# Kernel tuning notes

Hardware: AMD Instinct MI355X
Metric: run time of the kernel (lower is better)

Reference implementation:

```python
import jax, jax.numpy as jnp
import numpy as np

TAU = 0.5

def setup_inputs() -> dict:
    key = jax.random.key(0)
    ks = jax.random.split(key, 8)
    B_Nq, B_Ns, C, H, W = 16, 16, 512, 32, 32
    f_q = jax.random.normal(ks[0], (B_Nq, C, H, W), dtype=jnp.float32)
    f_s = jax.random.normal(ks[1], (B_Ns, C, H, W), dtype=jnp.float32)
    # depthwise 1x1 convs with groups=dim, bias=False -> per-channel scalar weights [C]
    w_cca_q = jax.random.normal(ks[2], (C,), dtype=jnp.float32)
    w_cca_k = jax.random.normal(ks[3], (C,), dtype=jnp.float32)
    w_cca_v = jax.random.normal(ks[4], (C,), dtype=jnp.float32)
    w_sca_q = jax.random.normal(ks[5], (C,), dtype=jnp.float32)
    w_sca_k = jax.random.normal(ks[6], (C,), dtype=jnp.float32)
    lam = jnp.float32(0.1)
    return {"f_q": f_q, "f_s": f_s, "w_cca_q": w_cca_q, "w_cca_k": w_cca_k,
            "w_cca_v": w_cca_v, "w_sca_q": w_sca_q, "w_sca_k": w_sca_k, "lam": lam}

def _dw(x, w):
    # depthwise 1x1 conv, no bias == per-channel scale; x: [B,C,H,W], w: [C]
    return x * w[None, :, None, None]

def reference(f_q, f_s, w_cca_q, w_cca_k, w_cca_v, w_sca_q, w_sca_k, lam):
    B_Nq, C, H, W = f_q.shape
    B_Ns = f_s.shape[0]
    P = H * W
    qc = _dw(f_q, w_cca_q).reshape(B_Nq, C, P)          # [B,C,P]
    kc_mean = _dw(f_s, w_cca_k).reshape(B_Ns, C, P).mean(axis=0)  # [C,P]
    vc_mean = _dw(f_s, w_cca_v).reshape(B_Ns, C, P).mean(axis=0)  # [C,P]
    # channel attention: [B,C,C]
    Ac = jax.nn.softmax(jnp.einsum('bcp,dp->bcd', qc, kc_mean) / P, axis=-1)
    f_cca_q = jnp.einsum('bcd,dp->bcp', Ac, vc_mean).reshape(B_Nq, C, H, W)
    qs = _dw(f_cca_q, w_sca_q).reshape(B_Nq, C, P)      # [B,C,P]
    ks_mean = _dw(f_s, w_sca_k).reshape(B_Ns, C, P).mean(axis=0)  # [C,P]
    # spatial affinity: [B,P,P]
    M = jnp.einsum('bcp,cq->bpq', qs, ks_mean) / (TAU * C)
    alpha = jax.nn.softmax(M.mean(axis=-1), axis=-1)    # [B_Nq,P]
    beta = jax.nn.softmax(M.mean(axis=-2), axis=-1)     # [B_Nq,P]
    beta_mean = jnp.broadcast_to(beta.mean(axis=0, keepdims=True), (B_Ns, P))
    Fq_out = f_q + lam * f_cca_q
    return (Fq_out, alpha, beta_mean)
```

## Files before the change

### kernel.cpp

```cpp
#include <hip/hip_runtime.h>

typedef __bf16 bf16;
typedef __bf16 bf16x4 __attribute__((ext_vector_type(4)));
typedef __bf16 bf16x8 __attribute__((ext_vector_type(8)));
typedef float f32x4 __attribute__((ext_vector_type(4)));


#define GLL16(g, l)                                                             \
    __builtin_amdgcn_global_load_lds((const __attribute__((address_space(1))) void*)(g), \
                                     (__attribute__((address_space(3))) void*)(l), 16, 0, 0)

__device__ inline float wave_reduce_sum(float v) {
#pragma unroll
    for (int m = 32; m >= 1; m >>= 1) v += __shfl_xor(v, m, 64);
    return v;
}
__device__ inline float wave_reduce_max(float v) {
#pragma unroll
    for (int m = 32; m >= 1; m >>= 1) v = fmaxf(v, __shfl_xor(v, m, 64));
    return v;
}

__global__ void k_prep(const float* __restrict__ fs, const float* __restrict__ fq,
                       float* __restrict__ fsm32, bf16* __restrict__ fsm16,
                       bf16* __restrict__ fsmT, bf16* __restrict__ fq16) {
    __shared__ bf16 tile[32][33];
    int bx = blockIdx.x, by = blockIdx.y;
    int p0 = bx * 32, c0 = by * 32;
    int t = threadIdx.x, tx = t & 31, ty = t >> 5;
#pragma unroll
    for (int i = 0; i < 4; ++i) {
        size_t off = (size_t)(c0 + ty + 8 * i) * 1024 + p0 + tx;
        float s = 0.f;
#pragma unroll
        for (int b = 0; b < 16; ++b) s += fs[(size_t)b * 524288 + off];
        s *= (1.f / 16.f);
        fsm32[off] = s;
        bf16 h = (bf16)s;
        fsm16[off] = h;
        tile[ty + 8 * i][tx] = h;
    }
    __syncthreads();
#pragma unroll
    for (int i = 0; i < 4; ++i)
        fsmT[(size_t)(p0 + ty + 8 * i) * 512 + c0 + tx] = tile[tx][ty + 8 * i];
    int blk = by * 32 + bx;
    const float4* f4 = (const float4*)fq;
#pragma unroll
    for (int i = 0; i < 16; ++i) {
        int idx = blk * 4096 + i * 256 + t;
        float4 v = f4[idx];
        bf16x4 h4 = {(bf16)v.x, (bf16)v.y, (bf16)v.z, (bf16)v.w};
        *(bf16x4*)(fq16 + (size_t)idx * 4) = h4;
    }
}

__global__ void k_u(const float* __restrict__ fsm32, const float* __restrict__ wsq,
                    const float* __restrict__ wsk, float* __restrict__ u,
                    float* __restrict__ rm) {
    int c = blockIdx.x;
    int t = threadIdx.x;
    float s = 0.f;
#pragma unroll
    for (int j = 0; j < 4; ++j) s += fsm32[(size_t)c * 1024 + t + 256 * j];
    s = wave_reduce_sum(s);
    __shared__ float red[4];
    int w = t >> 6, lane = t & 63;
    if (lane == 0) red[w] = s;
    __syncthreads();
    if (t == 0) {
        float rmv = (red[0] + red[1] + red[2] + red[3]) * (1.f / 1024.f);
        rm[c] = rmv;
        u[c] = wsq[c] * wsk[c] * rmv * (1.f / 256.f);
    }
}

__global__ void k_gemm1(const bf16* __restrict__ A, const bf16* __restrict__ B,
                        float* __restrict__ G) {
    __shared__ alignas(16) bf16 As[64 * 32];
    __shared__ alignas(16) bf16 Bs[128 * 32];
    const int dt = blockIdx.x, ct = blockIdx.y, b = blockIdx.z;
    const int t = threadIdx.x, w = t >> 6, lane = t & 63;
    const int quad = lane >> 4, r15 = lane & 15;
    const bf16* Abase = A + ((size_t)(b * 512 + ct * 64)) * 1024;
    const bf16* Bbase = B + ((size_t)(dt * 128)) * 1024;
    const int sr = t >> 2, sc = (t & 3) * 8;
    f32x4 acc[8] = {};
    for (int k0 = 0; k0 < 1024; k0 += 32) {
        GLL16(Abase + (size_t)sr * 1024 + k0 + sc, As + t * 8);
        GLL16(Bbase + (size_t)sr * 1024 + k0 + sc, Bs + t * 8);
        GLL16(Bbase + (size_t)(sr + 64) * 1024 + k0 + sc, Bs + (t + 256) * 8);
        __syncthreads();
        bf16x8 af = *(const bf16x8*)(As + (w * 16 + r15) * 32 + quad * 8);
#pragma unroll
        for (int j = 0; j < 8; ++j) {
            bf16x8 bfr = *(const bf16x8*)(Bs + (j * 16 + r15) * 32 + quad * 8);
            acc[j] = __builtin_amdgcn_mfma_f32_16x16x32_bf16(af, bfr, acc[j], 0, 0, 0);
        }
        __syncthreads();
    }
    float* g = G + ((size_t)(b * 512 + ct * 64 + w * 16 + quad * 4)) * 512 + dt * 128 + r15;
#pragma unroll
    for (int j = 0; j < 8; ++j)
#pragma unroll
        for (int ii = 0; ii < 4; ++ii)
            g[(size_t)ii * 512 + j * 16] = acc[j][ii];
}

__global__ void k_softmax_ac(const float* __restrict__ G, const float* __restrict__ wq,
                             const float* __restrict__ wk, const float* __restrict__ wv,
                             const float* __restrict__ rm, bf16* __restrict__ Acw,
                             float* __restrict__ r) {
    int row = blockIdx.x * 4 + (threadIdx.x >> 6);
    int lane = threadIdx.x & 63;
    int c = row & 511;
    const float* g = G + (size_t)row * 512;
    float sc = wq[c] * (1.f / 1024.f);
    float v[8];
    float mx = -3.4e38f;
#pragma unroll
    for (int j = 0; j < 8; ++j) {
        int d = lane + 64 * j;
        v[j] = g[d] * sc * wk[d];
        mx = fmaxf(mx, v[j]);
    }
    mx = wave_reduce_max(mx);
    float sum = 0.f;
#pragma unroll
    for (int j = 0; j < 8; ++j) {
        v[j] = __expf(v[j] - mx);
        sum += v[j];
    }
    sum = wave_reduce_sum(sum);
    float inv = 1.f / sum;
    bf16* o = Acw + (size_t)row * 512;
    float rsum = 0.f;
#pragma unroll
    for (int j = 0; j < 8; ++j) {
        int d = lane + 64 * j;
        float aw = v[j] * inv * wv[d];
        o[d] = (bf16)aw;
        rsum += aw * rm[d];
    }
    rsum = wave_reduce_sum(rsum);
    if (lane == 0) r[row] = rsum;
}

__global__ void k_t(const bf16* __restrict__ Acw, const float* __restrict__ u,
                    float* __restrict__ tbp) {
    int half = blockIdx.z, b = blockIdx.y;
    int d = blockIdx.x * 256 + threadIdx.x;
    const bf16* base = Acw + (size_t)b * 262144 + (size_t)half * 256 * 512 + d;
    const float* uu = u + half * 256;
    float s = 0.f;
#pragma unroll 16
    for (int c = 0; c < 256; ++c) s += uu[c] * (float)base[(size_t)c * 512];
    tbp[(half * 16 + b) * 512 + d] = s;
}

__global__ void k_gemm2(const bf16* __restrict__ A, const bf16* __restrict__ B,
                        const float* __restrict__ fq, const float* __restrict__ lamp,
                        float* __restrict__ out) {
    __shared__ alignas(16) bf16 As[64 * 32];
    __shared__ alignas(16) bf16 Bs[128 * 32];
    const int pt = blockIdx.x, ct = blockIdx.y, b = blockIdx.z;
    const int t = threadIdx.x, w = t >> 6, lane = t & 63;
    const int quad = lane >> 4, r15 = lane & 15;
    const bf16* Abase = A + ((size_t)(b * 512 + ct * 64)) * 512;
    const bf16* Bbase = B + ((size_t)(pt * 128)) * 512;
    const int sr = t >> 2, sc = (t & 3) * 8;
    f32x4 acc[8] = {};
    for (int k0 = 0; k0 < 512; k0 += 32) {
        GLL16(Abase + (size_t)sr * 512 + k0 + sc, As + t * 8);
        GLL16(Bbase + (size_t)sr * 512 + k0 + sc, Bs + t * 8);
        GLL16(Bbase + (size_t)(sr + 64) * 512 + k0 + sc, Bs + (t + 256) * 8);
        __syncthreads();
        bf16x8 af = *(const bf16x8*)(As + (w * 16 + r15) * 32 + quad * 8);
#pragma unroll
        for (int j = 0; j < 8; ++j) {
            bf16x8 bfr = *(const bf16x8*)(Bs + (j * 16 + r15) * 32 + quad * 8);
            acc[j] = __builtin_amdgcn_mfma_f32_16x16x32_bf16(af, bfr, acc[j], 0, 0, 0);
        }
        __syncthreads();
    }
    float lam = lamp[0];
    size_t rowbase = (size_t)(b * 512 + ct * 64 + w * 16 + quad * 4);
#pragma unroll
    for (int j = 0; j < 8; ++j)
#pragma unroll
        for (int ii = 0; ii < 4; ++ii) {
            size_t idx = (rowbase + ii) * 1024 + pt * 128 + j * 16 + r15;
            out[idx] = fq[idx] + lam * acc[j][ii];
        }
}

__global__ void k_logits(const float* __restrict__ tbp, const float* __restrict__ r,
                         const float* __restrict__ wsq, const float* __restrict__ wsk,
                         const float* __restrict__ fsm32, float* __restrict__ alog,
                         float* __restrict__ blog) {
    int z = blockIdx.y, pq = blockIdx.x * 256 + threadIdx.x;
    if (z < 16) {
        const float* t0 = tbp + z * 512;
        const float* t1 = tbp + (16 + z) * 512;
        float s = 0.f;
#pragma unroll 8
        for (int d = 0; d < 512; ++d) s += (t0[d] + t1[d]) * fsm32[(size_t)d * 1024 + pq];
        alog[z * 1024 + pq] = s;
    } else {
        int b = z - 16;
        float s = 0.f;
#pragma unroll 8
        for (int c = 0; c < 512; ++c) {
            float coef = r[b * 512 + c] * wsq[c] * wsk[c] * (1.f / 256.f);
            s += coef * fsm32[(size_t)c * 1024 + pq];
        }
        blog[b * 1024 + pq] = s;
    }
}

__global__ void k_softmax_rows(const float* __restrict__ alog, const float* __restrict__ blog,
                               float* __restrict__ alpha_out, float* __restrict__ beta) {
    int z = blockIdx.x;
    int t = threadIdx.x;
    int w = t >> 6, lane = t & 63;
    const float* src = (z < 16) ? (alog + (size_t)z * 1024) : (blog + (size_t)(z - 16) * 1024);
    float v[4];
    float mx = -3.4e38f;
#pragma unroll
    for (int j = 0; j < 4; ++j) {
        v[j] = src[t + 256 * j];
        mx = fmaxf(mx, v[j]);
    }
    __shared__ float red[4];
    float wm = wave_reduce_max(mx);
    if (lane == 0) red[w] = wm;
    __syncthreads();
    mx = fmaxf(fmaxf(red[0], red[1]), fmaxf(red[2], red[3]));
    float s = 0.f;
#pragma unroll
    for (int j = 0; j < 4; ++j) {
        v[j] = __expf(v[j] - mx);
        s += v[j];
    }
    __syncthreads();
    float ws_ = wave_reduce_sum(s);
    if (lane == 0) red[w] = ws_;
    __syncthreads();
    s = red[0] + red[1] + red[2] + red[3];
    float inv = 1.f / s;
    if (z < 16) {
#pragma unroll
        for (int j = 0; j < 4; ++j) alpha_out[(size_t)z * 1024 + t + 256 * j] = v[j] * inv;
    } else {
#pragma unroll
        for (int j = 0; j < 4; ++j) beta[(size_t)(z - 16) * 1024 + t + 256 * j] = v[j] * inv;
    }
}

__global__ void k_betamean(const float* __restrict__ beta, float* __restrict__ out) {
    int q = blockIdx.x * 256 + threadIdx.x;
    float s = 0.f;
#pragma unroll
    for (int b = 0; b < 16; ++b) s += beta[b * 1024 + q];
    float val = s * (1.f / 16.f);
#pragma unroll
    for (int si = 0; si < 16; ++si) out[(size_t)si * 1024 + q] = val;
}

extern "C" void kernel_launch(void* const* d_in, const int* in_sizes, int n_in,
                              void* d_out, int out_size, void* d_ws, size_t ws_size,
                              hipStream_t stream) {
    const float* f_q = (const float*)d_in[0];
    const float* f_s = (const float*)d_in[1];
    const float* w_cca_q = (const float*)d_in[2];
    const float* w_cca_k = (const float*)d_in[3];
    const float* w_cca_v = (const float*)d_in[4];
    const float* w_sca_q = (const float*)d_in[5];
    const float* w_sca_k = (const float*)d_in[6];
    const float* lamp = (const float*)d_in[7];

    char* ws = (char*)d_ws;
    float* fsm32 = (float*)(ws + 0);
    bf16* fsm16 = (bf16*)(ws + 2097152);
    bf16* fsmT = (bf16*)(ws + 3145728);
    float* G = (float*)(ws + 4194304);
    bf16* Acw = (bf16*)(ws + 20971520);
    bf16* fq16 = (bf16*)(ws + 29360128);
    float* rm = (float*)(ws + 46137344);
    float* u = (float*)(ws + 46139392);
    float* r = (float*)(ws + 46141440);
    float* tbp = (float*)(ws + 46174208);
    float* alog = (float*)(ws + 46239744);
    float* blog = (float*)(ws + 46305280);
    float* beta = (float*)(ws + 46370816);

    float* out_fq = (float*)d_out;
    float* out_alpha = out_fq + 8388608;
    float* out_bmean = out_fq + 8404992;

    k_prep<<<dim3(32, 16), 256, 0, stream>>>(f_s, f_q, fsm32, fsm16, fsmT, fq16);
    k_u<<<512, 256, 0, stream>>>(fsm32, w_sca_q, w_sca_k, u, rm);
    k_gemm1<<<dim3(4, 8, 16), 256, 0, stream>>>(fq16, fsm16, G);
    k_softmax_ac<<<2048, 256, 0, stream>>>(G, w_cca_q, w_cca_k, w_cca_v, rm, Acw, r);
    k_t<<<dim3(2, 16, 2), 256, 0, stream>>>(Acw, u, tbp);
    k_gemm2<<<dim3(8, 8, 16), 256, 0, stream>>>(Acw, fsmT, f_q, lamp, out_fq);
    k_logits<<<dim3(4, 32), 256, 0, stream>>>(tbp, r, w_sca_q, w_sca_k, fsm32, alog, blog);
    k_softmax_rows<<<32, 256, 0, stream>>>(alog, blog, out_alpha, beta);
    k_betamean<<<4, 256, 0, stream>>>(beta, out_bmean);
}
```

Before: 204.6 us.

## Fuse f_q bf16 conversion into gemm1 load and merge logits with softmax

Removes the separate pass converting f_q to bf16 in the prep kernel; gemm1 now loads fp32 f_q and converts to bf16 when writing to shared memory. The logits computation and row softmax are merged into one kernel using a shared coefficient vector, removing the intermediate logit buffers and a launch. This trades more fp32 global reads in gemm1 (synchronous loads instead of async LDS loads) and less parallelism in the logits stage for less memory traffic overall.

```diff
diff --git a/kernel.cpp b/kernel.cpp
--- a/kernel.cpp
+++ b/kernel.cpp
@@ -1,7 +1,6 @@
 #include <hip/hip_runtime.h>
 
 typedef __bf16 bf16;
-typedef __bf16 bf16x4 __attribute__((ext_vector_type(4)));
 typedef __bf16 bf16x8 __attribute__((ext_vector_type(8)));
 typedef float f32x4 __attribute__((ext_vector_type(4)));
 
@@ -21,12 +20,10 @@
     return v;
 }
 
-__global__ void k_prep(const float* __restrict__ fs, const float* __restrict__ fq,
-                       float* __restrict__ fsm32, bf16* __restrict__ fsm16,
-                       bf16* __restrict__ fsmT, bf16* __restrict__ fq16) {
+__global__ void k_prep(const float* __restrict__ fs, float* __restrict__ fsm32,
+                       bf16* __restrict__ fsm16, bf16* __restrict__ fsmT) {
     __shared__ bf16 tile[32][33];
-    int bx = blockIdx.x, by = blockIdx.y;
-    int p0 = bx * 32, c0 = by * 32;
+    int p0 = blockIdx.x * 32, c0 = blockIdx.y * 32;
     int t = threadIdx.x, tx = t & 31, ty = t >> 5;
 #pragma unroll
     for (int i = 0; i < 4; ++i) {
@@ -44,15 +41,6 @@
 #pragma unroll
     for (int i = 0; i < 4; ++i)
         fsmT[(size_t)(p0 + ty + 8 * i) * 512 + c0 + tx] = tile[tx][ty + 8 * i];
-    int blk = by * 32 + bx;
-    const float4* f4 = (const float4*)fq;
-#pragma unroll
-    for (int i = 0; i < 16; ++i) {
-        int idx = blk * 4096 + i * 256 + t;
-        float4 v = f4[idx];
-        bf16x4 h4 = {(bf16)v.x, (bf16)v.y, (bf16)v.z, (bf16)v.w};
-        *(bf16x4*)(fq16 + (size_t)idx * 4) = h4;
-    }
 }
 
 __global__ void k_u(const float* __restrict__ fsm32, const float* __restrict__ wsq,
@@ -75,21 +63,25 @@
     }
 }
 
-__global__ void k_gemm1(const bf16* __restrict__ A, const bf16* __restrict__ B,
+__global__ void k_gemm1(const float* __restrict__ A, const bf16* __restrict__ B,
                         float* __restrict__ G) {
     __shared__ alignas(16) bf16 As[64 * 32];
     __shared__ alignas(16) bf16 Bs[128 * 32];
     const int dt = blockIdx.x, ct = blockIdx.y, b = blockIdx.z;
     const int t = threadIdx.x, w = t >> 6, lane = t & 63;
     const int quad = lane >> 4, r15 = lane & 15;
-    const bf16* Abase = A + ((size_t)(b * 512 + ct * 64)) * 1024;
+    const float* Abase = A + ((size_t)(b * 512 + ct * 64)) * 1024;
     const bf16* Bbase = B + ((size_t)(dt * 128)) * 1024;
     const int sr = t >> 2, sc = (t & 3) * 8;
     f32x4 acc[8] = {};
     for (int k0 = 0; k0 < 1024; k0 += 32) {
-        GLL16(Abase + (size_t)sr * 1024 + k0 + sc, As + t * 8);
+        float4 a0 = *(const float4*)(Abase + (size_t)sr * 1024 + k0 + sc);
+        float4 a1 = *(const float4*)(Abase + (size_t)sr * 1024 + k0 + sc + 4);
         GLL16(Bbase + (size_t)sr * 1024 + k0 + sc, Bs + t * 8);
         GLL16(Bbase + (size_t)(sr + 64) * 1024 + k0 + sc, Bs + (t + 256) * 8);
+        bf16x8 ah = {(bf16)a0.x, (bf16)a0.y, (bf16)a0.z, (bf16)a0.w,
+                     (bf16)a1.x, (bf16)a1.y, (bf16)a1.z, (bf16)a1.w};
+        *(bf16x8*)(As + sr * 32 + sc) = ah;
         __syncthreads();
         bf16x8 af = *(const bf16x8*)(As + (w * 16 + r15) * 32 + quad * 8);
 #pragma unroll
@@ -194,44 +186,38 @@
         }
 }
 
-__global__ void k_logits(const float* __restrict__ tbp, const float* __restrict__ r,
-                         const float* __restrict__ wsq, const float* __restrict__ wsk,
-                         const float* __restrict__ fsm32, float* __restrict__ alog,
-                         float* __restrict__ blog) {
-    int z = blockIdx.y, pq = blockIdx.x * 256 + threadIdx.x;
-    if (z < 16) {
-        const float* t0 = tbp + z * 512;
-        const float* t1 = tbp + (16 + z) * 512;
-        float s = 0.f;
-#pragma unroll 8
-        for (int d = 0; d < 512; ++d) s += (t0[d] + t1[d]) * fsm32[(size_t)d * 1024 + pq];
-        alog[z * 1024 + pq] = s;
-    } else {
-        int b = z - 16;
-        float s = 0.f;
-#pragma unroll 8
-        for (int c = 0; c < 512; ++c) {
-            float coef = r[b * 512 + c] * wsq[c] * wsk[c] * (1.f / 256.f);
-            s += coef * fsm32[(size_t)c * 1024 + pq];
-        }
-        blog[b * 1024 + pq] = s;
-    }
-}
-
-__global__ void k_softmax_rows(const float* __restrict__ alog, const float* __restrict__ blog,
-                               float* __restrict__ alpha_out, float* __restrict__ beta) {
+__global__ void k_logsoft(const float* __restrict__ tbp, const float* __restrict__ r,
+                          const float* __restrict__ wsq, const float* __restrict__ wsk,
+                          const float* __restrict__ fsm32, float* __restrict__ alpha_out,
+                          float* __restrict__ beta) {
+    __shared__ float coef[512];
+    __shared__ float red[4];
     int z = blockIdx.x;
     int t = threadIdx.x;
     int w = t >> 6, lane = t & 63;
-    const float* src = (z < 16) ? (alog + (size_t)z * 1024) : (blog + (size_t)(z - 16) * 1024);
-    float v[4];
-    float mx = -3.4e38f;
-#pragma unroll
-    for (int j = 0; j < 4; ++j) {
-        v[j] = src[t + 256 * j];
-        mx = fmaxf(mx, v[j]);
-    }
-    __shared__ float red[4];
+    if (z < 16) {
+#pragma unroll
+        for (int j = 0; j < 2; ++j) {
+            int d = t + 256 * j;
+            coef[d] = tbp[z * 512 + d] + tbp[(16 + z) * 512 + d];
+        }
+    } else {
+        int b = z - 16;
+#pragma unroll
+        for (int j = 0; j < 2; ++j) {
+            int c = t + 256 * j;
+            coef[c] = r[b * 512 + c] * wsq[c] * wsk[c] * (1.f / 256.f);
+        }
+    }
+    __syncthreads();
+    float v[4] = {0.f, 0.f, 0.f, 0.f};
+    for (int d = 0; d < 512; ++d) {
+        float cv = coef[d];
+        const float* row = fsm32 + (size_t)d * 1024 + t;
+#pragma unroll
+        for (int j = 0; j < 4; ++j) v[j] = fmaf(cv, row[256 * j], v[j]);
+    }
+    float mx = fmaxf(fmaxf(v[0], v[1]), fmaxf(v[2], v[3]));
     float wm = wave_reduce_max(mx);
     if (lane == 0) red[w] = wm;
     __syncthreads();
@@ -285,26 +271,22 @@
     bf16* fsmT = (bf16*)(ws + 3145728);
     float* G = (float*)(ws + 4194304);
     bf16* Acw = (bf16*)(ws + 20971520);
-    bf16* fq16 = (bf16*)(ws + 29360128);
-    float* rm = (float*)(ws + 46137344);
-    float* u = (float*)(ws + 46139392);
-    float* r = (float*)(ws + 46141440);
-    float* tbp = (float*)(ws + 46174208);
-    float* alog = (float*)(ws + 46239744);
-    float* blog = (float*)(ws + 46305280);
-    float* beta = (float*)(ws + 46370816);
+    float* rm = (float*)(ws + 29360128);
+    float* u = (float*)(ws + 29362176);
+    float* r = (float*)(ws + 29364224);
+    float* tbp = (float*)(ws + 29396992);
+    float* beta = (float*)(ws + 29462528);
 
     float* out_fq = (float*)d_out;
     float* out_alpha = out_fq + 8388608;
     float* out_bmean = out_fq + 8404992;
 
-    k_prep<<<dim3(32, 16), 256, 0, stream>>>(f_s, f_q, fsm32, fsm16, fsmT, fq16);
+    k_prep<<<dim3(32, 16), 256, 0, stream>>>(f_s, fsm32, fsm16, fsmT);
     k_u<<<512, 256, 0, stream>>>(fsm32, w_sca_q, w_sca_k, u, rm);
-    k_gemm1<<<dim3(4, 8, 16), 256, 0, stream>>>(fq16, fsm16, G);
+    k_gemm1<<<dim3(4, 8, 16), 256, 0, stream>>>(f_q, fsm16, G);
     k_softmax_ac<<<2048, 256, 0, stream>>>(G, w_cca_q, w_cca_k, w_cca_v, rm, Acw, r);
     k_t<<<dim3(2, 16, 2), 256, 0, stream>>>(Acw, u, tbp);
     k_gemm2<<<dim3(8, 8, 16), 256, 0, stream>>>(Acw, fsmT, f_q, lamp, out_fq);
-    k_logits<<<dim3(4, 32), 256, 0, stream>>>(tbp, r, w_sca_q, w_sca_k, fsm32, alog, blog);
-    k_softmax_rows<<<32, 256, 0, stream>>>(alog, blog, out_alpha, beta);
+    k_logsoft<<<32, 256, 0, stream>>>(tbp, r, w_sca_q, w_sca_k, fsm32, out_alpha, beta);
     k_betamean<<<4, 256, 0, stream>>>(beta, out_bmean);
 }
```

Measured after the change: 225.8 us. 1.1x slower.

## Replace LDS-staged GEMM tiles with direct register loads and software prefetch

Applied to the files above, without the earlier changes.

Both GEMM kernels stop staging A and B tiles through shared memory with global_load_lds and two barriers per k-step. Each lane now loads its MFMA fragments straight from global memory into registers and prefetches the next k-slice of B and the slice after next of A, so loads overlap the MFMAs and no barriers are needed. The cost is that the B tile is no longer shared across the four waves: every wave fetches it separately, which quadruples B traffic through L1/L2, and register pressure rises from holding 16 bf16x8 B fragments.

```diff
diff --git a/kernel.cpp b/kernel.cpp
--- a/kernel.cpp
+++ b/kernel.cpp
@@ -5,10 +5,6 @@
 typedef __bf16 bf16x8 __attribute__((ext_vector_type(8)));
 typedef float f32x4 __attribute__((ext_vector_type(4)));
 
-
-#define GLL16(g, l)                                                             \
-    __builtin_amdgcn_global_load_lds((const __attribute__((address_space(1))) void*)(g), \
-                                     (__attribute__((address_space(3))) void*)(l), 16, 0, 0)
 
 __device__ inline float wave_reduce_sum(float v) {
 #pragma unroll
@@ -77,27 +73,30 @@
 
 __global__ void k_gemm1(const bf16* __restrict__ A, const bf16* __restrict__ B,
                         float* __restrict__ G) {
-    __shared__ alignas(16) bf16 As[64 * 32];
-    __shared__ alignas(16) bf16 Bs[128 * 32];
     const int dt = blockIdx.x, ct = blockIdx.y, b = blockIdx.z;
     const int t = threadIdx.x, w = t >> 6, lane = t & 63;
     const int quad = lane >> 4, r15 = lane & 15;
-    const bf16* Abase = A + ((size_t)(b * 512 + ct * 64)) * 1024;
-    const bf16* Bbase = B + ((size_t)(dt * 128)) * 1024;
-    const int sr = t >> 2, sc = (t & 3) * 8;
+    const bf16* ap = A + ((size_t)(b * 512 + ct * 64 + w * 16 + r15)) * 1024 + quad * 8;
+    const bf16* bp = B + ((size_t)(dt * 128 + r15)) * 1024 + quad * 8;
     f32x4 acc[8] = {};
+    bf16x8 a0 = *(const bf16x8*)ap;
+    bf16x8 a1 = *(const bf16x8*)(ap + 32);
+    bf16x8 bb[8], nb[8];
+#pragma unroll
+    for (int j = 0; j < 8; ++j) bb[j] = *(const bf16x8*)(bp + (size_t)j * 16384);
     for (int k0 = 0; k0 < 1024; k0 += 32) {
-        GLL16(Abase + (size_t)sr * 1024 + k0 + sc, As + t * 8);
-        GLL16(Bbase + (size_t)sr * 1024 + k0 + sc, Bs + t * 8);
-        GLL16(Bbase + (size_t)(sr + 64) * 1024 + k0 + sc, Bs + (t + 256) * 8);
-        __syncthreads();
-        bf16x8 af = *(const bf16x8*)(As + (w * 16 + r15) * 32 + quad * 8);
-#pragma unroll
-        for (int j = 0; j < 8; ++j) {
-            bf16x8 bfr = *(const bf16x8*)(Bs + (j * 16 + r15) * 32 + quad * 8);
-            acc[j] = __builtin_amdgcn_mfma_f32_16x16x32_bf16(af, bfr, acc[j], 0, 0, 0);
-        }
-        __syncthreads();
+        int kb = (k0 + 32 <= 992) ? k0 + 32 : 992;
+        int ka = (k0 + 64 <= 992) ? k0 + 64 : 992;
+        bf16x8 a2 = *(const bf16x8*)(ap + ka);
+#pragma unroll
+        for (int j = 0; j < 8; ++j) nb[j] = *(const bf16x8*)(bp + (size_t)j * 16384 + kb);
+#pragma unroll
+        for (int j = 0; j < 8; ++j)
+            acc[j] = __builtin_amdgcn_mfma_f32_16x16x32_bf16(a0, bb[j], acc[j], 0, 0, 0);
+        a0 = a1;
+        a1 = a2;
+#pragma unroll
+        for (int j = 0; j < 8; ++j) bb[j] = nb[j];
     }
     float* g = G + ((size_t)(b * 512 + ct * 64 + w * 16 + quad * 4)) * 512 + dt * 128 + r15;
 #pragma unroll
@@ -161,27 +160,30 @@
 __global__ void k_gemm2(const bf16* __restrict__ A, const bf16* __restrict__ B,
                         const float* __restrict__ fq, const float* __restrict__ lamp,
                         float* __restrict__ out) {
-    __shared__ alignas(16) bf16 As[64 * 32];
-    __shared__ alignas(16) bf16 Bs[128 * 32];
     const int pt = blockIdx.x, ct = blockIdx.y, b = blockIdx.z;
     const int t = threadIdx.x, w = t >> 6, lane = t & 63;
     const int quad = lane >> 4, r15 = lane & 15;
-    const bf16* Abase = A + ((size_t)(b * 512 + ct * 64)) * 512;
-    const bf16* Bbase = B + ((size_t)(pt * 128)) * 512;
-    const int sr = t >> 2, sc = (t & 3) * 8;
+    const bf16* ap = A + ((size_t)(b * 512 + ct * 64 + w * 16 + r15)) * 512 + quad * 8;
+    const bf16* bp = B + ((size_t)(pt * 128 + r15)) * 512 + quad * 8;
     f32x4 acc[8] = {};
+    bf16x8 a0 = *(const bf16x8*)ap;
+    bf16x8 a1 = *(const bf16x8*)(ap + 32);
+    bf16x8 bb[8], nb[8];
+#pragma unroll
+    for (int j = 0; j < 8; ++j) bb[j] = *(const bf16x8*)(bp + (size_t)j * 8192);
     for (int k0 = 0; k0 < 512; k0 += 32) {
-        GLL16(Abase + (size_t)sr * 512 + k0 + sc, As + t * 8);
-        GLL16(Bbase + (size_t)sr * 512 + k0 + sc, Bs + t * 8);
-        GLL16(Bbase + (size_t)(sr + 64) * 512 + k0 + sc, Bs + (t + 256) * 8);
-        __syncthreads();
-        bf16x8 af = *(const bf16x8*)(As + (w * 16 + r15) * 32 + quad * 8);
-#pragma unroll
-        for (int j = 0; j < 8; ++j) {
-            bf16x8 bfr = *(const bf16x8*)(Bs + (j * 16 + r15) * 32 + quad * 8);
-            acc[j] = __builtin_amdgcn_mfma_f32_16x16x32_bf16(af, bfr, acc[j], 0, 0, 0);
-        }
-        __syncthreads();
+        int kb = (k0 + 32 <= 480) ? k0 + 32 : 480;
+        int ka = (k0 + 64 <= 480) ? k0 + 64 : 480;
+        bf16x8 a2 = *(const bf16x8*)(ap + ka);
+#pragma unroll
+        for (int j = 0; j < 8; ++j) nb[j] = *(const bf16x8*)(bp + (size_t)j * 8192 + kb);
+#pragma unroll
+        for (int j = 0; j < 8; ++j)
+            acc[j] = __builtin_amdgcn_mfma_f32_16x16x32_bf16(a0, bb[j], acc[j], 0, 0, 0);
+        a0 = a1;
+        a1 = a2;
+#pragma unroll
+        for (int j = 0; j < 8; ++j) bb[j] = nb[j];
     }
     float lam = lamp[0];
     size_t rowbase = (size_t)(b * 512 + ct * 64 + w * 16 + quad * 4);
```

New measurement: 301.7 us. 1.47x slower.

## Double-buffer LDS in both GEMMs with XOR swizzle, smaller N tiles, split k_t four ways

Applied to the files above, without the earlier changes.

Both MFMA GEMMs now double-buffer their LDS tiles. The next K-slice is issued with global_load_lds before computing on the current one, and one barrier per iteration is dropped. The LDS column index is XOR-swizzled to cut bank conflicts, and the N tile is halved from 128 to 64, doubling the grid for more occupancy and parallelism. k_t is split into four channel quarters instead of two, and k_logits sums the four partials, so the workspace offsets move. In exchange there is less register reuse per block and more blocks re-reading the A tiles.

```diff
diff --git a/kernel.cpp b/kernel.cpp
--- a/kernel.cpp
+++ b/kernel.cpp
@@ -77,31 +77,37 @@
 
 __global__ void k_gemm1(const bf16* __restrict__ A, const bf16* __restrict__ B,
                         float* __restrict__ G) {
-    __shared__ alignas(16) bf16 As[64 * 32];
-    __shared__ alignas(16) bf16 Bs[128 * 32];
+    __shared__ alignas(16) bf16 As[2][64 * 32];
+    __shared__ alignas(16) bf16 Bs[2][64 * 32];
     const int dt = blockIdx.x, ct = blockIdx.y, b = blockIdx.z;
     const int t = threadIdx.x, w = t >> 6, lane = t & 63;
     const int quad = lane >> 4, r15 = lane & 15;
     const bf16* Abase = A + ((size_t)(b * 512 + ct * 64)) * 1024;
-    const bf16* Bbase = B + ((size_t)(dt * 128)) * 1024;
-    const int sr = t >> 2, sc = (t & 3) * 8;
-    f32x4 acc[8] = {};
+    const bf16* Bbase = B + ((size_t)(dt * 64)) * 1024;
+    const int sr = t >> 2;
+    const int gc = ((t & 3) ^ ((sr >> 1) & 3)) * 8;
+    const int rsel = (quad ^ ((r15 >> 1) & 3)) * 8;
+    f32x4 acc[4] = {};
+    GLL16(Abase + (size_t)sr * 1024 + gc, As[0] + t * 8);
+    GLL16(Bbase + (size_t)sr * 1024 + gc, Bs[0] + t * 8);
+    int cur = 0;
     for (int k0 = 0; k0 < 1024; k0 += 32) {
-        GLL16(Abase + (size_t)sr * 1024 + k0 + sc, As + t * 8);
-        GLL16(Bbase + (size_t)sr * 1024 + k0 + sc, Bs + t * 8);
-        GLL16(Bbase + (size_t)(sr + 64) * 1024 + k0 + sc, Bs + (t + 256) * 8);
         __syncthreads();
-        bf16x8 af = *(const bf16x8*)(As + (w * 16 + r15) * 32 + quad * 8);
-#pragma unroll
-        for (int j = 0; j < 8; ++j) {
-            bf16x8 bfr = *(const bf16x8*)(Bs + (j * 16 + r15) * 32 + quad * 8);
+        if (k0 + 32 < 1024) {
+            GLL16(Abase + (size_t)sr * 1024 + k0 + 32 + gc, As[cur ^ 1] + t * 8);
+            GLL16(Bbase + (size_t)sr * 1024 + k0 + 32 + gc, Bs[cur ^ 1] + t * 8);
+        }
+        bf16x8 af = *(const bf16x8*)(As[cur] + (w * 16 + r15) * 32 + rsel);
+#pragma unroll
+        for (int j = 0; j < 4; ++j) {
+            bf16x8 bfr = *(const bf16x8*)(Bs[cur] + (j * 16 + r15) * 32 + rsel);
             acc[j] = __builtin_amdgcn_mfma_f32_16x16x32_bf16(af, bfr, acc[j], 0, 0, 0);
         }
-        __syncthreads();
-    }
-    float* g = G + ((size_t)(b * 512 + ct * 64 + w * 16 + quad * 4)) * 512 + dt * 128 + r15;
-#pragma unroll
-    for (int j = 0; j < 8; ++j)
+        cur ^= 1;
+    }
+    float* g = G + ((size_t)(b * 512 + ct * 64 + w * 16 + quad * 4)) * 512 + dt * 64 + r15;
+#pragma unroll
+    for (int j = 0; j < 4; ++j)
 #pragma unroll
         for (int ii = 0; ii < 4; ++ii)
             g[(size_t)ii * 512 + j * 16] = acc[j][ii];
@@ -148,48 +154,54 @@
 
 __global__ void k_t(const bf16* __restrict__ Acw, const float* __restrict__ u,
                     float* __restrict__ tbp) {
-    int half = blockIdx.z, b = blockIdx.y;
+    int q = blockIdx.z, b = blockIdx.y;
     int d = blockIdx.x * 256 + threadIdx.x;
-    const bf16* base = Acw + (size_t)b * 262144 + (size_t)half * 256 * 512 + d;
-    const float* uu = u + half * 256;
+    const bf16* base = Acw + (size_t)b * 262144 + (size_t)q * 128 * 512 + d;
+    const float* uu = u + q * 128;
     float s = 0.f;
 #pragma unroll 16
-    for (int c = 0; c < 256; ++c) s += uu[c] * (float)base[(size_t)c * 512];
-    tbp[(half * 16 + b) * 512 + d] = s;
+    for (int c = 0; c < 128; ++c) s += uu[c] * (float)base[(size_t)c * 512];
+    tbp[(q * 16 + b) * 512 + d] = s;
 }
 
 __global__ void k_gemm2(const bf16* __restrict__ A, const bf16* __restrict__ B,
                         const float* __restrict__ fq, const float* __restrict__ lamp,
                         float* __restrict__ out) {
-    __shared__ alignas(16) bf16 As[64 * 32];
-    __shared__ alignas(16) bf16 Bs[128 * 32];
+    __shared__ alignas(16) bf16 As[2][64 * 32];
+    __shared__ alignas(16) bf16 Bs[2][64 * 32];
     const int pt = blockIdx.x, ct = blockIdx.y, b = blockIdx.z;
     const int t = threadIdx.x, w = t >> 6, lane = t & 63;
     const int quad = lane >> 4, r15 = lane & 15;
     const bf16* Abase = A + ((size_t)(b * 512 + ct * 64)) * 512;
-    const bf16* Bbase = B + ((size_t)(pt * 128)) * 512;
-    const int sr = t >> 2, sc = (t & 3) * 8;
-    f32x4 acc[8] = {};
+    const bf16* Bbase = B + ((size_t)(pt * 64)) * 512;
+    const int sr = t >> 2;
+    const int gc = ((t & 3) ^ ((sr >> 1) & 3)) * 8;
+    const int rsel = (quad ^ ((r15 >> 1) & 3)) * 8;
+    f32x4 acc[4] = {};
+    GLL16(Abase + (size_t)sr * 512 + gc, As[0] + t * 8);
+    GLL16(Bbase + (size_t)sr * 512 + gc, Bs[0] + t * 8);
+    int cur = 0;
     for (int k0 = 0; k0 < 512; k0 += 32) {
-        GLL16(Abase + (size_t)sr * 512 + k0 + sc, As + t * 8);
-        GLL16(Bbase + (size_t)sr * 512 + k0 + sc, Bs + t * 8);
-        GLL16(Bbase + (size_t)(sr + 64) * 512 + k0 + sc, Bs + (t + 256) * 8);
         __syncthreads();
-        bf16x8 af = *(const bf16x8*)(As + (w * 16 + r15) * 32 + quad * 8);
-#pragma unroll
-        for (int j = 0; j < 8; ++j) {
-            bf16x8 bfr = *(const bf16x8*)(Bs + (j * 16 + r15) * 32 + quad * 8);
+        if (k0 + 32 < 512) {
+            GLL16(Abase + (size_t)sr * 512 + k0 + 32 + gc, As[cur ^ 1] + t * 8);
+            GLL16(Bbase + (size_t)sr * 512 + k0 + 32 + gc, Bs[cur ^ 1] + t * 8);
+        }
+        bf16x8 af = *(const bf16x8*)(As[cur] + (w * 16 + r15) * 32 + rsel);
+#pragma unroll
+        for (int j = 0; j < 4; ++j) {
+            bf16x8 bfr = *(const bf16x8*)(Bs[cur] + (j * 16 + r15) * 32 + rsel);
             acc[j] = __builtin_amdgcn_mfma_f32_16x16x32_bf16(af, bfr, acc[j], 0, 0, 0);
         }
-        __syncthreads();
+        cur ^= 1;
     }
     float lam = lamp[0];
     size_t rowbase = (size_t)(b * 512 + ct * 64 + w * 16 + quad * 4);
 #pragma unroll
-    for (int j = 0; j < 8; ++j)
+    for (int j = 0; j < 4; ++j)
 #pragma unroll
         for (int ii = 0; ii < 4; ++ii) {
-            size_t idx = (rowbase + ii) * 1024 + pt * 128 + j * 16 + r15;
+            size_t idx = (rowbase + ii) * 1024 + pt * 64 + j * 16 + r15;
             out[idx] = fq[idx] + lam * acc[j][ii];
         }
 }
@@ -201,10 +213,12 @@
     int z = blockIdx.y, pq = blockIdx.x * 256 + threadIdx.x;
     if (z < 16) {
         const float* t0 = tbp + z * 512;
-        const float* t1 = tbp + (16 + z) * 512;
         float s = 0.f;
 #pragma unroll 8
-        for (int d = 0; d < 512; ++d) s += (t0[d] + t1[d]) * fsm32[(size_t)d * 1024 + pq];
+        for (int d = 0; d < 512; ++d) {
+            float tv = t0[d] + t0[8192 + d] + t0[16384 + d] + t0[24576 + d];
+            s += tv * fsm32[(size_t)d * 1024 + pq];
+        }
         alog[z * 1024 + pq] = s;
     } else {
         int b = z - 16;
@@ -290,9 +304,9 @@
     float* u = (float*)(ws + 46139392);
     float* r = (float*)(ws + 46141440);
     float* tbp = (float*)(ws + 46174208);
-    float* alog = (float*)(ws + 46239744);
-    float* blog = (float*)(ws + 46305280);
-    float* beta = (float*)(ws + 46370816);
+    float* alog = (float*)(ws + 46305280);
+    float* blog = (float*)(ws + 46370816);
+    float* beta = (float*)(ws + 46436352);
 
     float* out_fq = (float*)d_out;
     float* out_alpha = out_fq + 8388608;
@@ -300,10 +314,10 @@
 
     k_prep<<<dim3(32, 16), 256, 0, stream>>>(f_s, f_q, fsm32, fsm16, fsmT, fq16);
     k_u<<<512, 256, 0, stream>>>(fsm32, w_sca_q, w_sca_k, u, rm);
-    k_gemm1<<<dim3(4, 8, 16), 256, 0, stream>>>(fq16, fsm16, G);
+    k_gemm1<<<dim3(8, 8, 16), 256, 0, stream>>>(fq16, fsm16, G);
     k_softmax_ac<<<2048, 256, 0, stream>>>(G, w_cca_q, w_cca_k, w_cca_v, rm, Acw, r);
-    k_t<<<dim3(2, 16, 2), 256, 0, stream>>>(Acw, u, tbp);
-    k_gemm2<<<dim3(8, 8, 16), 256, 0, stream>>>(Acw, fsmT, f_q, lamp, out_fq);
+    k_t<<<dim3(2, 16, 4), 256, 0, stream>>>(Acw, u, tbp);
+    k_gemm2<<<dim3(16, 8, 16), 256, 0, stream>>>(Acw, fsmT, f_q, lamp, out_fq);
     k_logits<<<dim3(4, 32), 256, 0, stream>>>(tbp, r, w_sca_q, w_sca_k, fsm32, alog, blog);
     k_softmax_rows<<<32, 256, 0, stream>>>(alog, blog, out_alpha, beta);
     k_betamean<<<4, 256, 0, stream>>>(beta, out_bmean);
```

New measurement: 211.8 us. 1.03x slower.
